# Optimization experiments

Hardware: AMD Instinct MI355X
Metric: run time of the kernel (lower is better)

## Reference

```python
import jax, jax.numpy as jnp
from jax import lax
import numpy as np

B, L, T = 128, 4096, 48


def setup_inputs() -> dict:
    key = jax.random.key(0)
    k1, k2 = jax.random.split(key)
    inputs = jax.random.normal(k1, (B, L, T), dtype=jnp.float32)
    # glorot_uniform init for [T, T] transition matrix
    limit = float(np.sqrt(6.0 / (T + T)))
    transition_params = jax.random.uniform(k2, (T, T), dtype=jnp.float32,
                                           minval=-limit, maxval=limit)
    return {"inputs": inputs, "transition_params": transition_params}


def crf_decode(potentials, transitions):
    # potentials: [B, Lp, T]; transitions: [T, T]
    first = potentials[:, 0, :]                       # [B, T]
    rest = jnp.swapaxes(potentials[:, 1:, :], 0, 1)   # [Lp-1, B, T]

    def fwd_step(state, emit):
        # state: [B, T] scores for previous tag; transitions[i, j]: i -> j
        scores = state[:, :, None] + transitions[None, :, :]  # [B, T, T]
        bp = jnp.argmax(scores, axis=1).astype(jnp.int32)     # [B, T]
        new_state = jnp.max(scores, axis=1) + emit            # [B, T]
        return new_state, bp

    last, bps = lax.scan(fwd_step, first, rest)  # bps: [Lp-1, B, T]
    last_tag = jnp.argmax(last, axis=-1).astype(jnp.int32)    # [B]
    best_score = jnp.max(last, axis=-1)                       # [B]

    def back_step(tag, bp):
        # tag: [B] tag at step t+1; bp: [B, T] backpointers into step t
        prev = jnp.take_along_axis(bp, tag[:, None], axis=1)[:, 0]
        return prev, prev

    _, tags_prefix = lax.scan(back_step, last_tag, bps, reverse=True)  # [Lp-1, B]
    tags = jnp.concatenate([tags_prefix, last_tag[None, :]], axis=0)   # [Lp, B]
    return jnp.swapaxes(tags, 0, 1), best_score


def reference(inputs, transition_params):
    pot = inputs[:, 1:-1, :]  # drop first/last positions, [B, L-2, T]
    tags_id, _ = crf_decode(pot, transition_params)
    return (pot, transition_params, tags_id)
```

## Files before the change

### kernel.cpp

```cpp
#include <hip/hip_runtime.h>
#include <stdint.h>

#define BATCH 128
#define LFULL 4096
#define TT 48
#define NPOT 4094
#define NBP  4093
#define SEG  64
#define NSEG 64
#define SLOT 192

__device__ __forceinline__ float maxtree48(const float* s) {
    float r[16];
#pragma unroll
    for (int j = 0; j < 16; ++j)
        r[j] = fmaxf(fmaxf(s[3*j], s[3*j+1]), s[3*j+2]);
#pragma unroll
    for (int j = 0; j < 8; ++j) r[j] = fmaxf(r[j], r[j+8]);
#pragma unroll
    for (int j = 0; j < 4; ++j) r[j] = fmaxf(r[j], r[j+4]);
    return fmaxf(fmaxf(r[0], r[1]), fmaxf(r[2], r[3]));
}

__global__ __launch_bounds__(64) void k_forward(const float* __restrict__ in,
                                                const float* __restrict__ trans,
                                                char* __restrict__ statesBase,
                                                unsigned char* __restrict__ bound) {
    const int b = blockIdx.x;
    const int lane = threadIdx.x;
    const int kk = (lane < TT) ? lane : 0;

    __shared__ float ldsT[TT * TT];
    __shared__ __align__(16) float lsbuf[2][TT];

    for (int i = lane; i < TT * TT; i += 64) ldsT[i] = trans[i];
    __syncthreads();

    float tcol[TT];
#pragma unroll
    for (int j = 0; j < TT; ++j) tcol[j] = ldsT[j * TT + kk];

    const float* inb = in + (size_t)b * (LFULL * TT);
    char* sb = statesBase + (size_t)b * NBP * SLOT;

    float sv[TT];
#pragma unroll
    for (int j = 0; j < TT; j += 4) {
        float4 v = *(const float4*)(inb + TT + j);
        sv[j] = v.x; sv[j+1] = v.y; sv[j+2] = v.z; sv[j+3] = v.w;
    }
    if (lane < TT) ((float*)sb)[lane] = inb[TT + lane];

    auto STEP = [&](int t, float e) {
        float s[TT];
#pragma unroll
        for (int j = 0; j < TT; ++j) s[j] = sv[j] + tcol[j];
        float m = maxtree48(s);
        float snew = m + e;
        int pp = t & 1;
        if (lane < TT) lsbuf[pp][lane] = snew;
        __syncthreads();
#pragma unroll
        for (int j = 0; j < TT; j += 4) {
            float4 v = *(const float4*)(&lsbuf[pp][j]);
            sv[j] = v.x; sv[j+1] = v.y; sv[j+2] = v.z; sv[j+3] = v.w;
        }
        if (t <= NBP - 1 && lane < TT)
            *(float*)(sb + (size_t)t * SLOT + (size_t)lane * 4) = snew;
    };

    auto LD = [&](int t) -> float {
        return (t <= NBP) ? inb[(size_t)(t + 1) * TT + kk] : 0.0f;
    };

    float e0 = LD(1), e1 = LD(2), e2 = LD(3), e3 = LD(4);
    int t = 1;
    for (; t + 3 <= NBP; t += 4) {
        STEP(t,     e0); e0 = LD(t + 4);
        STEP(t + 1, e1); e1 = LD(t + 5);
        STEP(t + 2, e2); e2 = LD(t + 6);
        STEP(t + 3, e3); e3 = LD(t + 7);
    }
    for (; t <= NBP; ++t) { STEP(t, e0); e0 = e1; e1 = e2; e2 = e3; }

    if (lane == 0) {
        float best = sv[0]; int bi = 0;
#pragma unroll
        for (int j = 1; j < TT; ++j) {
            if (sv[j] > best) { best = sv[j]; bi = j; }
        }
        bound[b * (NSEG + 1) + NSEG] = (unsigned char)bi;
    }
}

#define CHUNK 16
__global__ __launch_bounds__(256) void k_bp(const float* __restrict__ trans,
                                            char* __restrict__ statesBase) {
    const int lane = threadIdx.x & 63;
    const int wv = threadIdx.x >> 6;
    const int b = blockIdx.y * 4 + wv;
    const int i0 = blockIdx.x * CHUNK;
    const int kk = (lane < TT) ? lane : 0;

    __shared__ float ldsT[TT * TT];
    for (int i = threadIdx.x; i < TT * TT; i += 256) ldsT[i] = trans[i];
    __syncthreads();

    float tcol[TT];
#pragma unroll
    for (int j = 0; j < TT; ++j) tcol[j] = ldsT[j * TT + kk];

    char* sb = statesBase + (size_t)b * NBP * SLOT;

    for (int ii = 0; ii < CHUNK; ++ii) {
        int i = i0 + ii;
        if (i >= NBP) break;
        const float* sp = (const float*)(sb + (size_t)i * SLOT);
        float sv[TT];
#pragma unroll
        for (int j = 0; j < TT; j += 4) {
            float4 v = *(const float4*)(sp + j);
            sv[j] = v.x; sv[j+1] = v.y; sv[j+2] = v.z; sv[j+3] = v.w;
        }
        float best = sv[0] + tcol[0]; int bi = 0;
#pragma unroll
        for (int j = 1; j < TT; ++j) {
            float v = sv[j] + tcol[j];
            if (v > best) { best = v; bi = j; }
        }
        if (lane < TT)
            *(unsigned char*)(sb + (size_t)i * SLOT + lane) = (unsigned char)bi;
    }
}

__global__ __launch_bounds__(64) void k_compose(const char* __restrict__ statesBase,
                                                unsigned char* __restrict__ G) {
    const int s = blockIdx.x, b = blockIdx.y;
    const int i0 = s * SEG;
    const int cnt = (SEG < NBP - i0) ? SEG : (NBP - i0);
    const int lane = threadIdx.x;

    __shared__ unsigned char lbp[SEG * TT];
    const char* sb = statesBase + (size_t)b * NBP * SLOT;
    for (int ii = 0; ii < cnt; ++ii) {
        if (lane < 12)
            ((uint32_t*)lbp)[ii * 12 + lane] =
                *(const uint32_t*)(sb + (size_t)(i0 + ii) * SLOT + (size_t)lane * 4);
    }
    __syncthreads();

    if (lane < TT) {
        int M = lane;
        for (int ii = cnt - 1; ii >= 0; --ii) M = lbp[ii * TT + M];
        G[(b * NSEG + s) * TT + lane] = (unsigned char)M;
    }
}

__global__ void k_boundary(const unsigned char* __restrict__ G,
                           unsigned char* __restrict__ bound) {
    int b = threadIdx.x;
    int x = bound[b * (NSEG + 1) + NSEG];
    for (int s = NSEG - 1; s >= 0; --s) {
        x = G[(b * NSEG + s) * TT + x];
        bound[b * (NSEG + 1) + s] = x;
    }
}

__global__ __launch_bounds__(64) void k_fill(const char* __restrict__ statesBase,
                                             const unsigned char* __restrict__ bound,
                                             float* __restrict__ tags) {
    const int s = blockIdx.x, b = blockIdx.y;
    const int i0 = s * SEG;
    const int cnt = (SEG < NBP - i0) ? SEG : (NBP - i0);
    const int lane = threadIdx.x;

    __shared__ unsigned char lbp[SEG * TT];
    const char* sb = statesBase + (size_t)b * NBP * SLOT;
    for (int ii = 0; ii < cnt; ++ii) {
        if (lane < 12)
            ((uint32_t*)lbp)[ii * 12 + lane] =
                *(const uint32_t*)(sb + (size_t)(i0 + ii) * SLOT + (size_t)lane * 4);
    }
    __syncthreads();

    if (lane == 0) {
        int x = bound[b * (NSEG + 1) + s + 1];
        if (s == NSEG - 1)
            tags[(size_t)b * NPOT + (NPOT - 1)] = (float)x;
        for (int ii = cnt - 1; ii >= 0; --ii) {
            x = lbp[ii * TT + x];
            tags[(size_t)b * NPOT + i0 + ii] = (float)x;
        }
    }
}

__global__ __launch_bounds__(256) void k_copy(const float* __restrict__ in,
                                              const float* __restrict__ trans,
                                              float* __restrict__ out) {
    const int potN4 = (BATCH * NPOT * TT) / 4;
    const int rowN = NPOT * TT;
    int idx = blockIdx.x * 256 + threadIdx.x;
    if (idx < potN4) {
        int p4 = idx * 4;
        int b = p4 / rowN;
        int off = p4 - b * rowN;
        float4 v = *(const float4*)(in + (size_t)b * (LFULL * TT) + off + TT);
        *(float4*)(out + p4) = v;
    } else if (idx < potN4 + (TT * TT) / 4) {
        int q = idx - potN4;
        *(float4*)(out + (size_t)BATCH * NPOT * TT + (size_t)q * 4) =
            *(const float4*)(trans + (size_t)q * 4);
    }
}

extern "C" void kernel_launch(void* const* d_in, const int* in_sizes, int n_in,
                              void* d_out, int out_size, void* d_ws, size_t ws_size,
                              hipStream_t stream) {
    (void)in_sizes; (void)n_in; (void)d_ws; (void)ws_size; (void)out_size;

    const float* in = (const float*)d_in[0];
    const float* trans = (const float*)d_in[1];
    float* out = (float*)d_out;

    char* statesBase = (char*)d_out;
    unsigned char* bound = (unsigned char*)(out + (size_t)BATCH * NPOT * TT);
    unsigned char* G = (unsigned char*)(out + (size_t)BATCH * NPOT * TT + TT * TT);
    float* tags = out + (size_t)BATCH * NPOT * TT + TT * TT;

    k_forward <<<dim3(BATCH),        dim3(64),  0, stream>>>(in, trans, statesBase, bound);
    k_bp      <<<dim3(256, 32),      dim3(256), 0, stream>>>(trans, statesBase);
    k_compose <<<dim3(NSEG, BATCH),  dim3(64),  0, stream>>>(statesBase, G);
    k_boundary<<<dim3(1),            dim3(BATCH), 0, stream>>>(G, bound);
    k_fill    <<<dim3(NSEG, BATCH),  dim3(64),  0, stream>>>(statesBase, bound, tags);

    int total4 = (BATCH * NPOT * TT) / 4 + (TT * TT) / 4;
    k_copy    <<<dim3((total4 + 255) / 256), dim3(256), 0, stream>>>(in, trans, out);
}
```

Before: 1.179 ms.

## Interleave two batch rows per wave in forward Viterbi scan

The forward kernel now processes two batch rows per 64-lane block, alternating steps between them so their independent dependency chains can overlap latency. Block-level __syncthreads is replaced by wave barriers since each block is a single wave, and state is read back from LDS each step. This halves the number of blocks and doubles serial work per wave, trading occupancy for instruction-level overlap.

```diff
diff --git a/kernel.cpp b/kernel.cpp
--- a/kernel.cpp
+++ b/kernel.cpp
@@ -26,12 +26,14 @@
                                                 const float* __restrict__ trans,
                                                 char* __restrict__ statesBase,
                                                 unsigned char* __restrict__ bound) {
-    const int b = blockIdx.x;
     const int lane = threadIdx.x;
     const int kk = (lane < TT) ? lane : 0;
+    const int bA = blockIdx.x * 2;
+    const int bB = bA + 1;
 
     __shared__ float ldsT[TT * TT];
-    __shared__ __align__(16) float lsbuf[2][TT];
+    __shared__ __align__(16) float lsA[TT];
+    __shared__ __align__(16) float lsB[TT];
 
     for (int i = lane; i < TT * TT; i += 64) ldsT[i] = trans[i];
     __syncthreads();
@@ -40,56 +42,75 @@
 #pragma unroll
     for (int j = 0; j < TT; ++j) tcol[j] = ldsT[j * TT + kk];
 
-    const float* inb = in + (size_t)b * (LFULL * TT);
-    char* sb = statesBase + (size_t)b * NBP * SLOT;
-
-    float sv[TT];
-#pragma unroll
-    for (int j = 0; j < TT; j += 4) {
-        float4 v = *(const float4*)(inb + TT + j);
-        sv[j] = v.x; sv[j+1] = v.y; sv[j+2] = v.z; sv[j+3] = v.w;
-    }
-    if (lane < TT) ((float*)sb)[lane] = inb[TT + lane];
-
-    auto STEP = [&](int t, float e) {
-        float s[TT];
-#pragma unroll
-        for (int j = 0; j < TT; ++j) s[j] = sv[j] + tcol[j];
-        float m = maxtree48(s);
-        float snew = m + e;
-        int pp = t & 1;
-        if (lane < TT) lsbuf[pp][lane] = snew;
-        __syncthreads();
+    const float* inA = in + (size_t)bA * (LFULL * TT);
+    const float* inB = in + (size_t)bB * (LFULL * TT);
+    char* sA = statesBase + (size_t)bA * NBP * SLOT;
+    char* sB = statesBase + (size_t)bB * NBP * SLOT;
+
+    {
+        float s0 = inA[TT + kk];
+        if (lane < TT) { lsA[lane] = s0; ((float*)sA)[lane] = s0; }
+        s0 = inB[TT + kk];
+        if (lane < TT) { lsB[lane] = s0; ((float*)sB)[lane] = s0; }
+    }
+    __builtin_amdgcn_wave_barrier();
+
+    auto STEP = [&](float* __restrict__ ls, char* __restrict__ sb, int t, float e) {
+        float cand[TT];
 #pragma unroll
         for (int j = 0; j < TT; j += 4) {
-            float4 v = *(const float4*)(&lsbuf[pp][j]);
-            sv[j] = v.x; sv[j+1] = v.y; sv[j+2] = v.z; sv[j+3] = v.w;
-        }
-        if (t <= NBP - 1 && lane < TT)
-            *(float*)(sb + (size_t)t * SLOT + (size_t)lane * 4) = snew;
+            float4 v = *(const float4*)(&ls[j]);
+            cand[j]   = v.x + tcol[j];
+            cand[j+1] = v.y + tcol[j+1];
+            cand[j+2] = v.z + tcol[j+2];
+            cand[j+3] = v.w + tcol[j+3];
+        }
+        float snew = maxtree48(cand) + e;
+        __builtin_amdgcn_wave_barrier();
+        if (lane < TT) {
+            ls[lane] = snew;
+            if (t <= NBP - 1)
+                *(float*)(sb + (size_t)t * SLOT + (size_t)lane * 4) = snew;
+        }
+        __builtin_amdgcn_wave_barrier();
     };
 
-    auto LD = [&](int t) -> float {
-        return (t <= NBP) ? inb[(size_t)(t + 1) * TT + kk] : 0.0f;
+    auto LDA = [&](int t) -> float {
+        return (t <= NBP) ? inA[(size_t)(t + 1) * TT + kk] : 0.0f;
     };
-
-    float e0 = LD(1), e1 = LD(2), e2 = LD(3), e3 = LD(4);
+    auto LDB = [&](int t) -> float {
+        return (t <= NBP) ? inB[(size_t)(t + 1) * TT + kk] : 0.0f;
+    };
+
+    float a0 = LDA(1), a1 = LDA(2), a2 = LDA(3), a3 = LDA(4);
+    float b0 = LDB(1), b1 = LDB(2), b2 = LDB(3), b3 = LDB(4);
     int t = 1;
     for (; t + 3 <= NBP; t += 4) {
-        STEP(t,     e0); e0 = LD(t + 4);
-        STEP(t + 1, e1); e1 = LD(t + 5);
-        STEP(t + 2, e2); e2 = LD(t + 6);
-        STEP(t + 3, e3); e3 = LD(t + 7);
-    }
-    for (; t <= NBP; ++t) { STEP(t, e0); e0 = e1; e1 = e2; e2 = e3; }
+        STEP(lsA, sA, t,     a0); a0 = LDA(t + 4);
+        STEP(lsB, sB, t,     b0); b0 = LDB(t + 4);
+        STEP(lsA, sA, t + 1, a1); a1 = LDA(t + 5);
+        STEP(lsB, sB, t + 1, b1); b1 = LDB(t + 5);
+        STEP(lsA, sA, t + 2, a2); a2 = LDA(t + 6);
+        STEP(lsB, sB, t + 2, b2); b2 = LDB(t + 6);
+        STEP(lsA, sA, t + 3, a3); a3 = LDA(t + 7);
+        STEP(lsB, sB, t + 3, b3); b3 = LDB(t + 7);
+    }
+    for (; t <= NBP; ++t) {
+        STEP(lsA, sA, t, a0); a0 = a1; a1 = a2; a2 = a3;
+        STEP(lsB, sB, t, b0); b0 = b1; b1 = b2; b2 = b3;
+    }
 
     if (lane == 0) {
-        float best = sv[0]; int bi = 0;
-#pragma unroll
-        for (int j = 1; j < TT; ++j) {
-            if (sv[j] > best) { best = sv[j]; bi = j; }
-        }
-        bound[b * (NSEG + 1) + NSEG] = (unsigned char)bi;
+        float best = lsA[0]; int bi = 0;
+#pragma unroll
+        for (int j = 1; j < TT; ++j)
+            if (lsA[j] > best) { best = lsA[j]; bi = j; }
+        bound[bA * (NSEG + 1) + NSEG] = (unsigned char)bi;
+        best = lsB[0]; bi = 0;
+#pragma unroll
+        for (int j = 1; j < TT; ++j)
+            if (lsB[j] > best) { best = lsB[j]; bi = j; }
+        bound[bB * (NSEG + 1) + NSEG] = (unsigned char)bi;
     }
 }
 
@@ -227,7 +248,7 @@
     unsigned char* G = (unsigned char*)(out + (size_t)BATCH * NPOT * TT + TT * TT);
     float* tags = out + (size_t)BATCH * NPOT * TT + TT * TT;
 
-    k_forward <<<dim3(BATCH),        dim3(64),  0, stream>>>(in, trans, statesBase, bound);
+    k_forward <<<dim3(BATCH / 2),    dim3(64),  0, stream>>>(in, trans, statesBase, bound);
     k_bp      <<<dim3(256, 32),      dim3(256), 0, stream>>>(trans, statesBase);
     k_compose <<<dim3(NSEG, BATCH),  dim3(64),  0, stream>>>(statesBase, G);
     k_boundary<<<dim3(1),            dim3(BATCH), 0, stream>>>(G, bound);
```

Measured after the change: 1.990 ms. 68.8% more time.
